# Performance work log

Measured on AMD Instinct MI355X. Metric: run time of the kernel, lower is better.

The kernel has to match this reference:

```python
import jax, jax.numpy as jnp
import numpy as np

N = 25000   # nodes
E = 600000  # edges (multiple of 48)
IN, H, OUT = 128, 256, 128
SLOPE = 0.01  # LeakyReLU default negative_slope


def _lin(x, w, b):
    return x @ w.T + b


def _leaky(v):
    return jnp.where(v > 0, v, SLOPE * v)


def _sage(x, src, dst, lw, lb, rw):
    # PyG SAGEConv (aggr='mean', root_weight=True, normalize=False):
    # out = lin_l(mean_{j in N(i)} x_j) + lin_r(x_i)
    agg = jax.ops.segment_sum(x[src], dst, num_segments=N)
    deg = jax.ops.segment_sum(jnp.ones((src.shape[0],), x.dtype), dst, num_segments=N)
    mean = agg / jnp.maximum(deg, 1.0)[:, None]
    return mean @ lw.T + lb + x @ rw.T


def setup_inputs() -> dict:
    key = jax.random.key(0)
    ks = jax.random.split(key, 32)

    def w(k, o, i):
        return jax.random.normal(k, (o, i), jnp.float32) * (1.0 / np.sqrt(i))

    def b(k, o):
        return jax.random.normal(k, (o,), jnp.float32) * 0.01

    inp = {
        'x': jax.random.normal(ks[0], (N, IN), jnp.float32),
        'edge_index': jax.random.randint(ks[1], (2, E), 0, N, dtype=jnp.int32),
        'edge_attr': jax.random.normal(ks[2], (E, 1), jnp.float32),
        'batch': jnp.zeros((N,), jnp.int32),
        'prelin_w': w(ks[3], H, IN), 'prelin_b': b(ks[4], H),
        'conv1_lw': w(ks[5], H, H), 'conv1_lb': b(ks[6], H), 'conv1_rw': w(ks[7], H, H),
        'conv2_lw': w(ks[8], H, H), 'conv2_lb': b(ks[9], H), 'conv2_rw': w(ks[10], H, H),
        'conv3_lw': w(ks[11], OUT, H), 'conv3_lb': b(ks[12], OUT), 'conv3_rw': w(ks[13], OUT, H),
        'hh1_w': w(ks[14], H, H), 'hh1_b': b(ks[15], H),
        'hh2_w': w(ks[16], H, H), 'hh2_b': b(ks[17], H),
        'oo_w': w(ks[18], OUT, OUT), 'oo_b': b(ks[19], OUT),
        'lin96_w': w(ks[20], 1, 192), 'lin96_b': b(ks[21], 1),
        'lin32_w': w(ks[22], 1, 64), 'lin32_b': b(ks[23], 1),
    }
    return inp


def reference(x, edge_index, edge_attr, batch,
              prelin_w, prelin_b,
              conv1_lw, conv1_lb, conv1_rw,
              conv2_lw, conv2_lb, conv2_rw,
              conv3_lw, conv3_lb, conv3_rw,
              hh1_w, hh1_b, hh2_w, hh2_b,
              oo_w, oo_b, lin96_w, lin96_b, lin32_w, lin32_b):
    src, dst = edge_index[0], edge_index[1]
    h = jax.nn.relu(_lin(x, prelin_w, prelin_b))
    h = jax.nn.relu(_sage(h, src, dst, conv1_lw, conv1_lb, conv1_rw))
    h = _leaky(_lin(h, hh1_w, hh1_b))
    h = jax.nn.relu(_sage(h, src, dst, conv2_lw, conv2_lb, conv2_rw))
    h = _leaky(_lin(h, hh2_w, hh2_b))
    h = jax.nn.relu(_sage(h, src, dst, conv3_lw, conv3_lb, conv3_rw))
    h = _leaky(_lin(h, oo_w, oo_b))  # [N, 128]

    xl = h[src]  # edge_left  = edge_index[0]
    xr = h[dst]  # edge_right = edge_index[1]
    f96 = jnp.concatenate([xl[:, :96], xr[:, :96]], axis=1)  # [E, 192]
    f32 = jnp.concatenate([xl[:, 96:], xr[:, 96:]], axis=1)  # [E, 64]
    f96 = jax.nn.relu(_lin(f96, lin96_w, lin96_b))  # [E, 1]
    f32 = jax.nn.relu(_lin(f32, lin32_w, lin32_b))  # [E, 1]
    edge_out = f96 * edge_attr + f32                # [E, 1]
    edge_out = edge_out.reshape(-1, 48).mean(axis=1).reshape(-1, 1)  # [E/48, 1]
    return edge_out
```

## Files before the change

### kernel.cpp

```cpp
#include <hip/hip_runtime.h>
#include <hip/hip_bf16.h>

#define N_NODES 25000
#define N_EDGES 600000
#define ACT_NONE 0
#define ACT_RELU 1
#define ACT_LEAKY 2

typedef __bf16 bf16x8 __attribute__((ext_vector_type(8)));
typedef float f32x4 __attribute__((ext_vector_type(4)));
typedef unsigned short u16x8 __attribute__((ext_vector_type(8)));
typedef unsigned short u16x4 __attribute__((ext_vector_type(4)));
typedef short s16x4 __attribute__((ext_vector_type(4)));

__device__ __forceinline__ unsigned short f2bf(float x) {
    union { float f; unsigned int u; } v; v.f = x;
    unsigned int r = (v.u + 0x7fffu + ((v.u >> 16) & 1u)) >> 16;
    return (unsigned short)r;
}
__device__ __forceinline__ float bf2f(unsigned short b) {
    union { float f; unsigned int u; } v; v.u = ((unsigned int)b) << 16;
    return v.f;
}

__global__ __launch_bounds__(256) void hist_kernel(const int* __restrict__ dst,
                                                   int* __restrict__ deg, int E) {
    int e = blockIdx.x * 256 + threadIdx.x;
    if (e < E) atomicAdd(&deg[dst[e]], 1);
}

__global__ __launch_bounds__(1024) void scan_kernel(const int* __restrict__ deg,
                                                    int* __restrict__ off,
                                                    int* __restrict__ cursor, int n) {
    __shared__ int wsum[16];
    int t = threadIdx.x, w = t >> 6, l = t & 63;
    int carry = 0;
    for (int base = 0; base < n; base += 1024) {
        int v = (base + t < n) ? deg[base + t] : 0;
        int x = v;
        #pragma unroll
        for (int d = 1; d < 64; d <<= 1) {
            int y = __shfl_up(x, d);
            if (l >= d) x += y;
        }
        if (l == 63) wsum[w] = x;
        __syncthreads();
        if (w == 0 && l < 16) {
            int s = wsum[l];
            #pragma unroll
            for (int d = 1; d < 16; d <<= 1) {
                int y = __shfl_up(s, d);
                if (l >= d) s += y;
            }
            wsum[l] = s;
        }
        __syncthreads();
        int woff = (w > 0) ? wsum[w - 1] : 0;
        int excl = x + woff - v;
        if (base + t < n) {
            off[base + t] = carry + excl;
            cursor[base + t] = carry + excl;
        }
        int total = wsum[15];
        __syncthreads();
        carry += total;
    }
    if (t == 0) off[n] = carry;
}

__global__ __launch_bounds__(256) void scatter_kernel(const int* __restrict__ src,
                                                      const int* __restrict__ dst,
                                                      int* __restrict__ cursor,
                                                      int* __restrict__ csr_src, int E) {
    int e = blockIdx.x * 256 + threadIdx.x;
    if (e < E) {
        int d = dst[e];
        int pos = atomicAdd(&cursor[d], 1);
        csr_src[pos] = src[e];
    }
}

__global__ __launch_bounds__(256) void convert_kernel(const float* __restrict__ src,
                                                      unsigned short* __restrict__ hi,
                                                      unsigned short* __restrict__ lo, int n) {
    int i = blockIdx.x * 256 + threadIdx.x;
    if (i < n) {
        float x = src[i];
        unsigned short h = f2bf(x);
        hi[i] = h;
        lo[i] = f2bf(x - bf2f(h));
    }
}

struct CvtBatch {
    const float* src[10];
    unsigned short* hi[10];
    unsigned short* lo[10];
    int count[10];
};
__global__ __launch_bounds__(256) void convert_batch_kernel(CvtBatch b) {
    int seg = blockIdx.y;
    int n = b.count[seg];
    int i = blockIdx.x * 256 + threadIdx.x;
    if (i >= n) return;
    float x = b.src[seg][i];
    unsigned short h = f2bf(x);
    b.hi[seg][i] = h;
    b.lo[seg][i] = f2bf(x - bf2f(h));
}

__global__ __launch_bounds__(256) void quant_kernel(const float* __restrict__ h,
                                                    short* __restrict__ qt,
                                                    float* __restrict__ qscale) {
    int node = blockIdx.x * 4 + (threadIdx.x >> 6);
    if (node >= N_NODES) return;
    int lane = threadIdx.x & 63;
    long base = (long)node * 256 + (long)lane * 4;
    f32x4 v = *(const f32x4*)&h[base];
    float m = fmaxf(fmaxf(fabsf(v[0]), fabsf(v[1])), fmaxf(fabsf(v[2]), fabsf(v[3])));
    #pragma unroll
    for (int d = 32; d > 0; d >>= 1) m = fmaxf(m, __shfl_xor(m, d));
    float inv = (m > 0.0f) ? 32767.0f / m : 0.0f;
    float scale = (m > 0.0f) ? m / 32767.0f : 0.0f;
    s16x4 q;
    #pragma unroll
    for (int j = 0; j < 4; ++j) q[j] = (short)(int)rintf(v[j] * inv);
    *(s16x4*)&qt[base] = q;
    if (lane == 0) qscale[node] = scale;
}

__global__ __launch_bounds__(256) void sage_mean_kernel(const short* __restrict__ qt,
                                                        const float* __restrict__ qscale,
                                                        const int* __restrict__ off,
                                                        const int* __restrict__ csr_src,
                                                        unsigned short* __restrict__ mh,
                                                        unsigned short* __restrict__ ml) {
    int node = blockIdx.x * 4 + (threadIdx.x >> 6);
    if (node >= N_NODES) return;
    int lane = threadIdx.x & 63;
    int s0 = off[node], s1 = off[node + 1];
    f32x4 acc0 = {0.f, 0.f, 0.f, 0.f}, acc1 = {0.f, 0.f, 0.f, 0.f};
    f32x4 acc2 = {0.f, 0.f, 0.f, 0.f}, acc3 = {0.f, 0.f, 0.f, 0.f};
    long loff = (long)lane * 4;
    int e = s0;
    for (; e + 4 <= s1; e += 4) {
        int iA = csr_src[e], iB = csr_src[e + 1], iC = csr_src[e + 2], iD = csr_src[e + 3];
        s16x4 qa = *(const s16x4*)&qt[(long)iA * 256 + loff];
        s16x4 qb = *(const s16x4*)&qt[(long)iB * 256 + loff];
        s16x4 qc = *(const s16x4*)&qt[(long)iC * 256 + loff];
        s16x4 qd = *(const s16x4*)&qt[(long)iD * 256 + loff];
        float sa = qscale[iA], sb = qscale[iB], sc = qscale[iC], sd = qscale[iD];
        #pragma unroll
        for (int j = 0; j < 4; ++j) {
            acc0[j] += sa * (float)qa[j];
            acc1[j] += sb * (float)qb[j];
            acc2[j] += sc * (float)qc[j];
            acc3[j] += sd * (float)qd[j];
        }
    }
    for (; e < s1; ++e) {
        int iA = csr_src[e];
        s16x4 qa = *(const s16x4*)&qt[(long)iA * 256 + loff];
        float sa = qscale[iA];
        #pragma unroll
        for (int j = 0; j < 4; ++j) acc0[j] += sa * (float)qa[j];
    }
    float inv = 1.0f / fmaxf((float)(s1 - s0), 1.0f);
    f32x4 m = ((acc0 + acc1) + (acc2 + acc3)) * inv;
    u16x4 hb, lb;
    #pragma unroll
    for (int j = 0; j < 4; ++j) {
        unsigned short hv = f2bf(m[j]);
        hb[j] = hv;
        lb[j] = f2bf(m[j] - bf2f(hv));
    }
    long base = (long)node * 256 + loff;
    *(u16x4*)&mh[base] = hb;
    *(u16x4*)&ml[base] = lb;
}

__global__ __launch_bounds__(256, 2) void gemm_mfma_kernel(
    const unsigned short* __restrict__ A1h, const unsigned short* __restrict__ A1l,
    const unsigned short* __restrict__ W1h, const unsigned short* __restrict__ W1l,
    const unsigned short* __restrict__ A2h, const unsigned short* __restrict__ A2l,
    const unsigned short* __restrict__ W2h, const unsigned short* __restrict__ W2l,
    const float* __restrict__ bias,
    float* __restrict__ Cf, unsigned short* __restrict__ Ch, unsigned short* __restrict__ Cl,
    int M, int K, int O, int act)
{
    __shared__ unsigned short sAh[128][64];
    __shared__ unsigned short sAl[128][64];
    __shared__ unsigned short sWh[128][64];
    __shared__ unsigned short sWl[128][64];

    int tid = threadIdx.x;
    int row0 = blockIdx.x * 128;
    int col0 = blockIdx.y * 128;
    int wid = tid >> 6, lane = tid & 63;
    int wm = (wid >> 1) * 64, wo = (wid & 1) * 64;
    int fr = lane & 15, qk = lane >> 4;
    int rr = lane >> 3, qq = lane & 7;
    int shalf = (qq >> 2) * 32, scq = qq & 3;

    const int nt1 = K >> 6;
    const int nt  = (A2h != nullptr) ? (nt1 << 1) : nt1;

    f32x4 acc[4][4] = {};

    for (int t = 0; t < nt; ++t) {
        const unsigned short *Ah, *Al, *Wh, *Wl;
        int k0;
        if (t < nt1) { Ah = A1h; Al = A1l; Wh = W1h; Wl = W1l; k0 = t << 6; }
        else         { Ah = A2h; Al = A2l; Wh = W2h; Wl = W2l; k0 = (t - nt1) << 6; }

        #pragma unroll
        for (int i = 0; i < 4; ++i) {
            int rb = wid * 32 + i * 8;
            int r  = rb + rr;
            int gs = shalf + ((scq + (r >> 1)) & 3) * 8;
            long ar = (long)(row0 + r); if (ar > M - 1) ar = M - 1;
            long wr = (long)(col0 + r);
            __builtin_amdgcn_global_load_lds(
                (const __attribute__((address_space(1))) unsigned int*)(Ah + ar * K + k0 + gs),
                (__attribute__((address_space(3))) unsigned int*)&sAh[rb][0], 16, 0, 0);
            __builtin_amdgcn_global_load_lds(
                (const __attribute__((address_space(1))) unsigned int*)(Al + ar * K + k0 + gs),
                (__attribute__((address_space(3))) unsigned int*)&sAl[rb][0], 16, 0, 0);
            __builtin_amdgcn_global_load_lds(
                (const __attribute__((address_space(1))) unsigned int*)(Wh + wr * K + k0 + gs),
                (__attribute__((address_space(3))) unsigned int*)&sWh[rb][0], 16, 0, 0);
            __builtin_amdgcn_global_load_lds(
                (const __attribute__((address_space(1))) unsigned int*)(Wl + wr * K + k0 + gs),
                (__attribute__((address_space(3))) unsigned int*)&sWl[rb][0], 16, 0, 0);
        }
        __syncthreads();

        #pragma unroll
        for (int kk = 0; kk < 2; ++kk) {
            bf16x8 ah[4], al[4], bh[4], bl[4];
            #pragma unroll
            for (int i = 0; i < 4; ++i) {
                int rowA = wm + i * 16 + fr;
                int offA = rowA * 64 + kk * 32 + 8 * ((qk - (rowA >> 1)) & 3);
                ah[i] = *(const bf16x8*)(&sAh[0][0] + offA);
                al[i] = *(const bf16x8*)(&sAl[0][0] + offA);
                int rowB = wo + i * 16 + fr;
                int offB = rowB * 64 + kk * 32 + 8 * ((qk - (rowB >> 1)) & 3);
                bh[i] = *(const bf16x8*)(&sWh[0][0] + offB);
                bl[i] = *(const bf16x8*)(&sWl[0][0] + offB);
            }
            #pragma unroll
            for (int i = 0; i < 4; ++i) {
                #pragma unroll
                for (int j = 0; j < 4; ++j) {
                    acc[i][j] = __builtin_amdgcn_mfma_f32_16x16x32_bf16(ah[i], bh[j], acc[i][j], 0, 0, 0);
                    acc[i][j] = __builtin_amdgcn_mfma_f32_16x16x32_bf16(ah[i], bl[j], acc[i][j], 0, 0, 0);
                    acc[i][j] = __builtin_amdgcn_mfma_f32_16x16x32_bf16(al[i], bh[j], acc[i][j], 0, 0, 0);
                }
            }
        }
        __syncthreads();
    }

    int rgrp = (lane >> 4) * 4;
    int cl_ = lane & 15;
    #pragma unroll
    for (int i = 0; i < 4; ++i) {
        #pragma unroll
        for (int j = 0; j < 4; ++j) {
            int gcol = col0 + wo + j * 16 + cl_;
            float bv = bias[gcol];
            #pragma unroll
            for (int r = 0; r < 4; ++r) {
                int grow = row0 + wm + i * 16 + rgrp + r;
                if (grow < M) {
                    float v = acc[i][j][r] + bv;
                    if (act == ACT_RELU)       v = fmaxf(v, 0.0f);
                    else if (act == ACT_LEAKY) v = (v > 0.0f) ? v : 0.01f * v;
                    long idx = (long)grow * O + gcol;
                    if (Cf) Cf[idx] = v;
                    if (Ch) {
                        unsigned short hbits = f2bf(v);
                        Ch[idx] = hbits;
                        Cl[idx] = f2bf(v - bf2f(hbits));
                    }
                }
            }
        }
    }
}

__global__ __launch_bounds__(256) void node_dots_kernel(const float* __restrict__ h,
                                                        const float* __restrict__ w96,
                                                        const float* __restrict__ w32,
                                                        float* __restrict__ nodeDot) {
    int node = blockIdx.x * 4 + (threadIdx.x >> 6);
    if (node >= N_NODES) return;
    int lane = threadIdx.x & 63;
    const float* row = h + (long)node * 128;
    float h0 = row[lane];
    float h1 = row[64 + lane];
    float pL96 = h0 * w96[lane];
    float pR96 = h0 * w96[96 + lane];
    float pL32 = 0.0f, pR32 = 0.0f;
    if (lane < 32) {
        pL96 += h1 * w96[64 + lane];
        pR96 += h1 * w96[160 + lane];
    } else {
        int k = lane - 32;
        pL32 = h1 * w32[k];
        pR32 = h1 * w32[32 + k];
    }
    #pragma unroll
    for (int m = 32; m > 0; m >>= 1) {
        pL96 += __shfl_xor(pL96, m);
        pR96 += __shfl_xor(pR96, m);
        pL32 += __shfl_xor(pL32, m);
        pR32 += __shfl_xor(pR32, m);
    }
    if (lane == 0) {
        f32x4 v = {pL96, pR96, pL32, pR32};
        *(f32x4*)&nodeDot[(long)node * 4] = v;
    }
}

__global__ __launch_bounds__(256) void edge_group_kernel(const float* __restrict__ nodeDot,
                                                         const int* __restrict__ src,
                                                         const int* __restrict__ dst,
                                                         const float* __restrict__ eattr,
                                                         const float* __restrict__ b96,
                                                         const float* __restrict__ b32,
                                                         float* __restrict__ out, int G) {
    int g = blockIdx.x * 256 + threadIdx.x;
    if (g >= G) return;
    float bb96 = b96[0], bb32 = b32[0];
    int base = g * 48;
    float s = 0.0f;
    #pragma unroll 4
    for (int k = 0; k < 48; ++k) {
        int e = base + k;
        f32x4 a = *(const f32x4*)&nodeDot[(long)src[e] * 4];
        f32x4 b = *(const f32x4*)&nodeDot[(long)dst[e] * 4];
        float f96  = fmaxf(a[0] + b[1] + bb96, 0.0f);
        float f32v = fmaxf(a[2] + b[3] + bb32, 0.0f);
        s += f96 * eattr[e] + f32v;
    }
    out[g] = s * (1.0f / 48.0f);
}

extern "C" void kernel_launch(void* const* d_in, const int* in_sizes, int n_in,
                              void* d_out, int out_size, void* d_ws, size_t ws_size,
                              hipStream_t stream) {
    const float* x         = (const float*)d_in[0];
    const int*   edge_idx  = (const int*)d_in[1];
    const float* edge_attr = (const float*)d_in[2];
    const float* prelin_w  = (const float*)d_in[4];
    const float* prelin_b  = (const float*)d_in[5];
    const float* conv1_lw  = (const float*)d_in[6];
    const float* conv1_lb  = (const float*)d_in[7];
    const float* conv1_rw  = (const float*)d_in[8];
    const float* conv2_lw  = (const float*)d_in[9];
    const float* conv2_lb  = (const float*)d_in[10];
    const float* conv2_rw  = (const float*)d_in[11];
    const float* conv3_lw  = (const float*)d_in[12];
    const float* conv3_lb  = (const float*)d_in[13];
    const float* conv3_rw  = (const float*)d_in[14];
    const float* hh1_w     = (const float*)d_in[15];
    const float* hh1_b     = (const float*)d_in[16];
    const float* hh2_w     = (const float*)d_in[17];
    const float* hh2_b     = (const float*)d_in[18];
    const float* oo_w      = (const float*)d_in[19];
    const float* oo_b      = (const float*)d_in[20];
    const float* lin96_w   = (const float*)d_in[21];
    const float* lin96_b   = (const float*)d_in[22];
    const float* lin32_w   = (const float*)d_in[23];
    const float* lin32_b   = (const float*)d_in[24];

    const int* src = edge_idx;
    const int* dst = edge_idx + N_EDGES;

    char* wsp = (char*)d_ws;
    size_t used = 0;
    auto alloc = [&](size_t bytes) -> char* {
        char* r = wsp;
        size_t pad = (bytes + 255) & ~(size_t)255;
        wsp += pad; used += pad;
        return r;
    };
    float* bufF = (float*)alloc((size_t)N_NODES * 256 * 4);
    unsigned short* P0h = (unsigned short*)alloc((size_t)N_NODES * 256 * 2);
    unsigned short* P0l = (unsigned short*)alloc((size_t)N_NODES * 256 * 2);
    unsigned short* P1h = (unsigned short*)alloc((size_t)N_NODES * 256 * 2);
    unsigned short* P1l = (unsigned short*)alloc((size_t)N_NODES * 256 * 2);
    unsigned short* P2h = (unsigned short*)alloc((size_t)N_NODES * 256 * 2);
    unsigned short* P2l = (unsigned short*)alloc((size_t)N_NODES * 256 * 2);
    short* qtab    = (short*)alloc((size_t)N_NODES * 256 * 2);
    float* qscale  = (float*)alloc((size_t)N_NODES * 4);
    float* nodeDot = (float*)alloc((size_t)N_NODES * 4 * 4);
    int* deg       = (int*)alloc((size_t)N_NODES * 4);
    int* off       = (int*)alloc((size_t)(N_NODES + 1) * 4);
    int* cursor    = (int*)alloc((size_t)N_NODES * 4);
    int* csr_src   = (int*)alloc((size_t)N_EDGES * 4);

    struct WP { unsigned short *h, *l; };
    auto wpair = [&](int n) -> WP {
        WP w; w.h = (unsigned short*)alloc((size_t)n * 2);
        w.l = (unsigned short*)alloc((size_t)n * 2); return w;
    };
    WP w_pre = wpair(256 * 128);
    WP w_c1l = wpair(256 * 256), w_c1r = wpair(256 * 256);
    WP w_c2l = wpair(256 * 256), w_c2r = wpair(256 * 256);
    WP w_c3l = wpair(128 * 256), w_c3r = wpair(128 * 256);
    WP w_h1  = wpair(256 * 256), w_h2 = wpair(256 * 256);
    WP w_oo  = wpair(128 * 128);

    if (used > ws_size) return;

    const int EB = (N_EDGES + 255) / 256;
    const int MB = (N_NODES + 127) / 128;
    const int NB4 = (N_NODES + 3) / 4;

    (void)hipMemsetAsync(deg, 0, N_NODES * sizeof(int), stream);
    hist_kernel<<<EB, 256, 0, stream>>>(dst, deg, N_EDGES);
    scan_kernel<<<1, 1024, 0, stream>>>(deg, off, cursor, N_NODES);
    scatter_kernel<<<EB, 256, 0, stream>>>(src, dst, cursor, csr_src, N_EDGES);

    convert_kernel<<<((N_NODES * 128) + 255) / 256, 256, 0, stream>>>(x, P0h, P0l, N_NODES * 128);
    CvtBatch cb;
    const float* wsrc[10] = {prelin_w, conv1_lw, conv1_rw, conv2_lw, conv2_rw,
                             conv3_lw, conv3_rw, hh1_w, hh2_w, oo_w};
    WP wdst[10] = {w_pre, w_c1l, w_c1r, w_c2l, w_c2r, w_c3l, w_c3r, w_h1, w_h2, w_oo};
    int wcnt[10] = {256 * 128, 256 * 256, 256 * 256, 256 * 256, 256 * 256,
                    128 * 256, 128 * 256, 256 * 256, 256 * 256, 128 * 128};
    for (int i = 0; i < 10; ++i) {
        cb.src[i] = wsrc[i]; cb.hi[i] = wdst[i].h; cb.lo[i] = wdst[i].l; cb.count[i] = wcnt[i];
    }
    convert_batch_kernel<<<dim3((65536 + 255) / 256, 10), 256, 0, stream>>>(cb);

    gemm_mfma_kernel<<<dim3(MB, 2), 256, 0, stream>>>(
        P0h, P0l, w_pre.h, w_pre.l, nullptr, nullptr, nullptr, nullptr,
        prelin_b, bufF, P1h, P1l, N_NODES, 128, 256, ACT_RELU);

    quant_kernel<<<NB4, 256, 0, stream>>>(bufF, qtab, qscale);
    sage_mean_kernel<<<NB4, 256, 0, stream>>>(qtab, qscale, off, csr_src, P2h, P2l);
    gemm_mfma_kernel<<<dim3(MB, 2), 256, 0, stream>>>(
        P2h, P2l, w_c1l.h, w_c1l.l, P1h, P1l, w_c1r.h, w_c1r.l,
        conv1_lb, nullptr, P0h, P0l, N_NODES, 256, 256, ACT_RELU);
    gemm_mfma_kernel<<<dim3(MB, 2), 256, 0, stream>>>(
        P0h, P0l, w_h1.h, w_h1.l, nullptr, nullptr, nullptr, nullptr,
        hh1_b, bufF, P1h, P1l, N_NODES, 256, 256, ACT_LEAKY);

    quant_kernel<<<NB4, 256, 0, stream>>>(bufF, qtab, qscale);
    sage_mean_kernel<<<NB4, 256, 0, stream>>>(qtab, qscale, off, csr_src, P2h, P2l);
    gemm_mfma_kernel<<<dim3(MB, 2), 256, 0, stream>>>(
        P2h, P2l, w_c2l.h, w_c2l.l, P1h, P1l, w_c2r.h, w_c2r.l,
        conv2_lb, nullptr, P0h, P0l, N_NODES, 256, 256, ACT_RELU);
    gemm_mfma_kernel<<<dim3(MB, 2), 256, 0, stream>>>(
        P0h, P0l, w_h2.h, w_h2.l, nullptr, nullptr, nullptr, nullptr,
        hh2_b, bufF, P1h, P1l, N_NODES, 256, 256, ACT_LEAKY);

    quant_kernel<<<NB4, 256, 0, stream>>>(bufF, qtab, qscale);
    sage_mean_kernel<<<NB4, 256, 0, stream>>>(qtab, qscale, off, csr_src, P2h, P2l);
    gemm_mfma_kernel<<<dim3(MB, 1), 256, 0, stream>>>(
        P2h, P2l, w_c3l.h, w_c3l.l, P1h, P1l, w_c3r.h, w_c3r.l,
        conv3_lb, nullptr, P0h, P0l, N_NODES, 256, 128, ACT_RELU);
    gemm_mfma_kernel<<<dim3(MB, 1), 256, 0, stream>>>(
        P0h, P0l, w_oo.h, w_oo.l, nullptr, nullptr, nullptr, nullptr,
        oo_b, bufF, nullptr, nullptr, N_NODES, 128, 128, ACT_LEAKY);

    node_dots_kernel<<<NB4, 256, 0, stream>>>(bufF, lin96_w, lin32_w, nodeDot);
    const int G = N_EDGES / 48;
    edge_group_kernel<<<(G + 255) / 256, 256, 0, stream>>>(
        nodeDot, src, dst, edge_attr, lin96_b, lin32_b, (float*)d_out, G);
}
```

Measured before the change: 478.2 us.

## Fuse int16 quantization into GEMM epilogue with per-64-column scales

Removes the standalone quant kernel by quantizing activations to int16 inside the GEMM epilogue. Each 64-column quarter now gets its own scale, found with a 16-lane shuffle max-reduction, and sage_mean reads the per-quarter scale. The fp32 intermediate write and reread (bufF) is skipped for these layers, and three launches go away. The cost is extra shuffles in the epilogue and a finer scale granularity, which changes the quantization numerics slightly.

```diff
diff --git a/kernel.cpp b/kernel.cpp
--- a/kernel.cpp
+++ b/kernel.cpp
@@ -109,28 +109,8 @@
     b.lo[seg][i] = f2bf(x - bf2f(h));
 }
 
-__global__ __launch_bounds__(256) void quant_kernel(const float* __restrict__ h,
-                                                    short* __restrict__ qt,
-                                                    float* __restrict__ qscale) {
-    int node = blockIdx.x * 4 + (threadIdx.x >> 6);
-    if (node >= N_NODES) return;
-    int lane = threadIdx.x & 63;
-    long base = (long)node * 256 + (long)lane * 4;
-    f32x4 v = *(const f32x4*)&h[base];
-    float m = fmaxf(fmaxf(fabsf(v[0]), fabsf(v[1])), fmaxf(fabsf(v[2]), fabsf(v[3])));
-    #pragma unroll
-    for (int d = 32; d > 0; d >>= 1) m = fmaxf(m, __shfl_xor(m, d));
-    float inv = (m > 0.0f) ? 32767.0f / m : 0.0f;
-    float scale = (m > 0.0f) ? m / 32767.0f : 0.0f;
-    s16x4 q;
-    #pragma unroll
-    for (int j = 0; j < 4; ++j) q[j] = (short)(int)rintf(v[j] * inv);
-    *(s16x4*)&qt[base] = q;
-    if (lane == 0) qscale[node] = scale;
-}
-
 __global__ __launch_bounds__(256) void sage_mean_kernel(const short* __restrict__ qt,
-                                                        const float* __restrict__ qscale,
+                                                        const float* __restrict__ qs4,
                                                         const int* __restrict__ off,
                                                         const int* __restrict__ csr_src,
                                                         unsigned short* __restrict__ mh,
@@ -138,6 +118,7 @@
     int node = blockIdx.x * 4 + (threadIdx.x >> 6);
     if (node >= N_NODES) return;
     int lane = threadIdx.x & 63;
+    int qidx = lane >> 4;
     int s0 = off[node], s1 = off[node + 1];
     f32x4 acc0 = {0.f, 0.f, 0.f, 0.f}, acc1 = {0.f, 0.f, 0.f, 0.f};
     f32x4 acc2 = {0.f, 0.f, 0.f, 0.f}, acc3 = {0.f, 0.f, 0.f, 0.f};
@@ -149,7 +130,8 @@
         s16x4 qb = *(const s16x4*)&qt[(long)iB * 256 + loff];
         s16x4 qc = *(const s16x4*)&qt[(long)iC * 256 + loff];
         s16x4 qd = *(const s16x4*)&qt[(long)iD * 256 + loff];
-        float sa = qscale[iA], sb = qscale[iB], sc = qscale[iC], sd = qscale[iD];
+        float sa = qs4[(long)iA * 4 + qidx], sb = qs4[(long)iB * 4 + qidx];
+        float sc = qs4[(long)iC * 4 + qidx], sd = qs4[(long)iD * 4 + qidx];
         #pragma unroll
         for (int j = 0; j < 4; ++j) {
             acc0[j] += sa * (float)qa[j];
@@ -161,7 +143,7 @@
     for (; e < s1; ++e) {
         int iA = csr_src[e];
         s16x4 qa = *(const s16x4*)&qt[(long)iA * 256 + loff];
-        float sa = qscale[iA];
+        float sa = qs4[(long)iA * 4 + qidx];
         #pragma unroll
         for (int j = 0; j < 4; ++j) acc0[j] += sa * (float)qa[j];
     }
@@ -186,6 +168,7 @@
     const unsigned short* __restrict__ W2h, const unsigned short* __restrict__ W2l,
     const float* __restrict__ bias,
     float* __restrict__ Cf, unsigned short* __restrict__ Ch, unsigned short* __restrict__ Cl,
+    short* __restrict__ Cq, float* __restrict__ Cqs,
     int M, int K, int O, int act)
 {
     __shared__ unsigned short sAh[128][64];
@@ -264,28 +247,49 @@
 
     int rgrp = (lane >> 4) * 4;
     int cl_ = lane & 15;
+    int quarter = (col0 + wo) >> 6;
     #pragma unroll
     for (int i = 0; i < 4; ++i) {
-        #pragma unroll
-        for (int j = 0; j < 4; ++j) {
-            int gcol = col0 + wo + j * 16 + cl_;
-            float bv = bias[gcol];
+        float bv[4];
+        #pragma unroll
+        for (int j = 0; j < 4; ++j) bv[j] = bias[col0 + wo + j * 16 + cl_];
+        #pragma unroll
+        for (int r = 0; r < 4; ++r) {
+            int grow = row0 + wm + i * 16 + rgrp + r;
+            float vv[4];
+            float m = 0.0f;
             #pragma unroll
-            for (int r = 0; r < 4; ++r) {
-                int grow = row0 + wm + i * 16 + rgrp + r;
-                if (grow < M) {
-                    float v = acc[i][j][r] + bv;
-                    if (act == ACT_RELU)       v = fmaxf(v, 0.0f);
-                    else if (act == ACT_LEAKY) v = (v > 0.0f) ? v : 0.01f * v;
-                    long idx = (long)grow * O + gcol;
+            for (int j = 0; j < 4; ++j) {
+                float v = acc[i][j][r] + bv[j];
+                if (act == ACT_RELU)       v = fmaxf(v, 0.0f);
+                else if (act == ACT_LEAKY) v = (v > 0.0f) ? v : 0.01f * v;
+                vv[j] = v;
+                m = fmaxf(m, fabsf(v));
+            }
+            float qinv = 0.0f;
+            if (Cq) {
+                #pragma unroll
+                for (int d = 1; d < 16; d <<= 1) m = fmaxf(m, __shfl_xor(m, d));
+                qinv = (m > 0.0f) ? 32767.0f / m : 0.0f;
+            }
+            bool ok = grow < M;
+            #pragma unroll
+            for (int j = 0; j < 4; ++j) {
+                int gcol = col0 + wo + j * 16 + cl_;
+                long idx = (long)grow * O + gcol;
+                if (ok) {
+                    float v = vv[j];
                     if (Cf) Cf[idx] = v;
                     if (Ch) {
                         unsigned short hbits = f2bf(v);
                         Ch[idx] = hbits;
                         Cl[idx] = f2bf(v - bf2f(hbits));
                     }
+                    if (Cq) Cq[idx] = (short)(int)rintf(v * qinv);
                 }
             }
+            if (Cq && ok && cl_ == 0)
+                Cqs[(long)grow * 4 + quarter] = (m > 0.0f) ? m / 32767.0f : 0.0f;
         }
     }
 }
@@ -395,7 +399,7 @@
     unsigned short* P2h = (unsigned short*)alloc((size_t)N_NODES * 256 * 2);
     unsigned short* P2l = (unsigned short*)alloc((size_t)N_NODES * 256 * 2);
     short* qtab    = (short*)alloc((size_t)N_NODES * 256 * 2);
-    float* qscale  = (float*)alloc((size_t)N_NODES * 4);
+    float* qsc4    = (float*)alloc((size_t)N_NODES * 4 * 4);
     float* nodeDot = (float*)alloc((size_t)N_NODES * 4 * 4);
     int* deg       = (int*)alloc((size_t)N_NODES * 4);
     int* off       = (int*)alloc((size_t)(N_NODES + 1) * 4);
@@ -439,34 +443,31 @@
 
     gemm_mfma_kernel<<<dim3(MB, 2), 256, 0, stream>>>(
         P0h, P0l, w_pre.h, w_pre.l, nullptr, nullptr, nullptr, nullptr,
-        prelin_b, bufF, P1h, P1l, N_NODES, 128, 256, ACT_RELU);
-
-    quant_kernel<<<NB4, 256, 0, stream>>>(bufF, qtab, qscale);
-    sage_mean_kernel<<<NB4, 256, 0, stream>>>(qtab, qscale, off, csr_src, P2h, P2l);
+        prelin_b, nullptr, P1h, P1l, qtab, qsc4, N_NODES, 128, 256, ACT_RELU);
+
+    sage_mean_kernel<<<NB4, 256, 0, stream>>>(qtab, qsc4, off, csr_src, P2h, P2l);
     gemm_mfma_kernel<<<dim3(MB, 2), 256, 0, stream>>>(
         P2h, P2l, w_c1l.h, w_c1l.l, P1h, P1l, w_c1r.h, w_c1r.l,
-        conv1_lb, nullptr, P0h, P0l, N_NODES, 256, 256, ACT_RELU);
+        conv1_lb, nullptr, P0h, P0l, nullptr, nullptr, N_NODES, 256, 256, ACT_RELU);
     gemm_mfma_kernel<<<dim3(MB, 2), 256, 0, stream>>>(
         P0h, P0l, w_h1.h, w_h1.l, nullptr, nullptr, nullptr, nullptr,
-        hh1_b, bufF, P1h, P1l, N_NODES, 256, 256, ACT_LEAKY);
-
-    quant_kernel<<<NB4, 256, 0, stream>>>(bufF, qtab, qscale);
-    sage_mean_kernel<<<NB4, 256, 0, stream>>>(qtab, qscale, off, csr_src, P2h, P2l);
+        hh1_b, nullptr, P1h, P1l, qtab, qsc4, N_NODES, 256, 256, ACT_LEAKY);
+
+    sage_mean_kernel<<<NB4, 256, 0, stream>>>(qtab, qsc4, off, csr_src, P2h, P2l);
     gemm_mfma_kernel<<<dim3(MB, 2), 256, 0, stream>>>(
         P2h, P2l, w_c2l.h, w_c2l.l, P1h, P1l, w_c2r.h, w_c2r.l,
-        conv2_lb, nullptr, P0h, P0l, N_NODES, 256, 256, ACT_RELU);
+        conv2_lb, nullptr, P0h, P0l, nullptr, nullptr, N_NODES, 256, 256, ACT_RELU);
     gemm_mfma_kernel<<<dim3(MB, 2), 256, 0, stream>>>(
         P0h, P0l, w_h2.h, w_h2.l, nullptr, nullptr, nullptr, nullptr,
-        hh2_b, bufF, P1h, P1l, N_NODES, 256, 256, ACT_LEAKY);
-
-    quant_kernel<<<NB4, 256, 0, stream>>>(bufF, qtab, qscale);
-    sage_mean_kernel<<<NB4, 256, 0, stream>>>(qtab, qscale, off, csr_src, P2h, P2l);
+        hh2_b, nullptr, P1h, P1l, qtab, qsc4, N_NODES, 256, 256, ACT_LEAKY);
+
+    sage_mean_kernel<<<NB4, 256, 0, stream>>>(qtab, qsc4, off, csr_src, P2h, P2l);
     gemm_mfma_kernel<<<dim3(MB, 1), 256, 0, stream>>>(
         P2h, P2l, w_c3l.h, w_c3l.l, P1h, P1l, w_c3r.h, w_c3r.l,
-        conv3_lb, nullptr, P0h, P0l, N_NODES, 256, 128, ACT_RELU);
+        conv3_lb, nullptr, P0h, P0l, nullptr, nullptr, N_NODES, 256, 128, ACT_RELU);
     gemm_mfma_kernel<<<dim3(MB, 1), 256, 0, stream>>>(
         P0h, P0l, w_oo.h, w_oo.l, nullptr, nullptr, nullptr, nullptr,
-        oo_b, bufF, nullptr, nullptr, N_NODES, 128, 128, ACT_LEAKY);
+        oo_b, bufF, nullptr, nullptr, nullptr, nullptr, N_NODES, 128, 128, ACT_LEAKY);
 
     node_dots_kernel<<<NB4, 256, 0, stream>>>(bufF, lin96_w, lin32_w, nodeDot);
     const int G = N_EDGES / 48;
```

Result: faster. 441.0 us (-7.8%).
